# Kernel optimization log

Measured on AMD Instinct MI355X. Metric: run time of the kernel, lower is better.

The kernel has to match this reference:

```python
import jax, jax.numpy as jnp
import numpy as np

B, T, N, C, H = 32, 50, 1024, 128, 64


def setup_inputs() -> dict:
    key = jax.random.key(0)
    ks = jax.random.split(key, 5)
    s_ih = 1.0 / np.sqrt(H)
    return {
        "chars": jax.random.normal(ks[0], (B, T, N, C), dtype=jnp.float32),
        "W_ih": jax.random.uniform(ks[1], (3 * H, C), minval=-s_ih, maxval=s_ih, dtype=jnp.float32),
        "W_hh": jax.random.uniform(ks[2], (3 * H, H), minval=-s_ih, maxval=s_ih, dtype=jnp.float32),
        "b_ih": jax.random.uniform(ks[3], (3 * H,), minval=-s_ih, maxval=s_ih, dtype=jnp.float32),
        "b_hh": jax.random.uniform(ks[4], (3 * H,), minval=-s_ih, maxval=s_ih, dtype=jnp.float32),
    }


def _gru_scan(chars, W_ih, W_hh, b_ih, b_hh):
    b, t, n, c = chars.shape
    h_dim = W_hh.shape[1]
    # (B,T,N,C) -> (T, B*N, C): every (batch, stock) pair is an independent sequence
    x = jnp.transpose(chars, (1, 0, 2, 3)).reshape(t, b * n, c)
    # precompute input projections for all steps: (T, B*N, 3H)
    gi = jnp.einsum("tbc,gc->tbg", x, W_ih) + b_ih

    def step(h, gi_t):
        gh = h @ W_hh.T + b_hh                      # (B*N, 3H)
        i_r, i_z, i_n = jnp.split(gi_t, 3, axis=-1)
        h_r, h_z, h_n = jnp.split(gh, 3, axis=-1)
        r = jax.nn.sigmoid(i_r + h_r)
        z = jax.nn.sigmoid(i_z + h_z)
        nn_ = jnp.tanh(i_n + r * h_n)
        h_new = (1.0 - z) * nn_ + z * h
        return h_new, None

    h0 = jnp.zeros((b * n, h_dim), dtype=chars.dtype)
    h_final, _ = jax.lax.scan(step, h0, gi)
    return h_final.reshape(b, n, h_dim)


def reference(chars, W_ih, W_hh, b_ih, b_hh):
    return _gru_scan(chars, W_ih, W_hh, b_ih, b_hh)
```

## Files before the change

### kernel.cpp

```cpp
#include <hip/hip_runtime.h>


typedef _Float16 half8 __attribute__((ext_vector_type(8)));
typedef float f32x4 __attribute__((ext_vector_type(4)));

constexpr int T_ = 50, N_ = 1024, C_ = 128, H_ = 64;
constexpr uint32_t WHH_OFF = 0;
constexpr uint32_t XB_OFF  = 24576;
constexpr uint32_t HB_OFF  = 32768;
constexpr int LDS_BYTES = 36864;

__global__ void prep_weights(const float* __restrict__ Wih, const float* __restrict__ Whh,
                             _Float16* __restrict__ w16) {
  int i = blockIdx.x * 256 + threadIdx.x;
  if (i < 192 * 128) w16[i] = (_Float16)Wih[i];
  if (i < 192 * 64)  w16[24576 + i] = (_Float16)Whh[i];
}

__device__ __forceinline__ float sigm(float x) {
  return __builtin_amdgcn_rcpf(1.f + __expf(-x));
}

__device__ __forceinline__ half8 cvt8(float4 lo, float4 hi) {
  half8 v;
  v[0] = (_Float16)lo.x; v[1] = (_Float16)lo.y;
  v[2] = (_Float16)lo.z; v[3] = (_Float16)lo.w;
  v[4] = (_Float16)hi.x; v[5] = (_Float16)hi.y;
  v[6] = (_Float16)hi.z; v[7] = (_Float16)hi.w;
  return v;
}

__global__ __launch_bounds__(256, 4) void gru_g4(
    const float* __restrict__ x, const _Float16* __restrict__ w16,
    const float* __restrict__ bih, const float* __restrict__ bhh,
    float* __restrict__ out)
{
  __shared__ __align__(16) char lds[LDS_BYTES];
  const int tid = threadIdx.x;
  const int wv = tid >> 6, lane = tid & 63;
  const int c = lane & 15, g = lane >> 4;
  const int jt = wv;
  const int seq0 = blockIdx.x * 16;
  const int b = seq0 >> 10, n0 = seq0 & (N_ - 1);

  {
    const _Float16* whh = w16 + 24576;
#pragma unroll
    for (int rep = 0; rep < 6; ++rep) {
      int i = tid + rep * 256;
      int row = i >> 3, gr = i & 7;
      uint32_t byte = (uint32_t)row * 128 + (uint32_t)((gr ^ (row & 7)) << 4);
      *(half8*)(lds + WHH_OFF + byte) = *(const half8*)(whh + i * 8);
    }
    half8 zz = {};
    *(half8*)(lds + HB_OFF + tid * 16) = zz;
  }

  half8 wr[3][4];
#pragma unroll
  for (int gate = 0; gate < 3; ++gate)
#pragma unroll
    for (int ks = 0; ks < 4; ++ks)
      wr[gate][ks] = *(const half8*)(w16 + (gate * 64 + jt * 16 + c) * 128 + ks * 32 + g * 8);

  const int j = jt * 16 + c;
  const float br   = bih[j] + bhh[j];
  const float bz   = bih[64 + j] + bhh[64 + j];
  const float bin_ = bih[128 + j];
  const float bhn_ = bhh[128 + j];

  float hr[4] = {0.f, 0.f, 0.f, 0.f};

  const int sseq = tid >> 4;
  const uint32_t xw_off = (uint32_t)sseq * 256 +
                          (uint32_t)(((tid & 15) ^ (sseq & 7)) << 4);
  const float* xbase = x + ((size_t)b * T_ * N_ + n0 + sseq) * C_ + (tid & 15) * 8;
  const size_t stepstride = (size_t)N_ * C_;

#define WHHB(gate, ks2) \
  (*(const half8*)(lds + WHH_OFF + (uint32_t)(((gate) * 64 + jt * 16 + c) * 128) + \
                   (uint32_t)((((ks2) * 4 + g) ^ (c & 7)) << 4)))
#define MFMA16(a, bf, acc) __builtin_amdgcn_mfma_f32_16x16x32_f16((a), (bf), (acc), 0, 0, 0)

  {
    float4 r0 = *(const float4*)(xbase);
    float4 r1 = *(const float4*)(xbase + 4);
    *(half8*)(lds + XB_OFF + xw_off) = cvt8(r0, r1);
  }
  float4 ra = *(const float4*)(xbase + stepstride);
  float4 rb = *(const float4*)(xbase + stepstride + 4);
  __syncthreads();

  for (int t = 0; t < T_; ++t) {
    const uint32_t xr  = XB_OFF + (uint32_t)(t & 1) * 4096;
    const uint32_t hrd = HB_OFF + (uint32_t)((t + 1) & 1) * 2048;
    const uint32_t hwr = HB_OFF + (uint32_t)(t & 1) * 2048;

    half8 xa[4];
#pragma unroll
    for (int ks = 0; ks < 4; ++ks)
      xa[ks] = *(const half8*)(lds + xr + (uint32_t)c * 256 +
                               (uint32_t)(((ks * 4 + g) ^ (c & 7)) << 4));
    half8 ha[2];
#pragma unroll
    for (int ks2 = 0; ks2 < 2; ++ks2)
      ha[ks2] = *(const half8*)(lds + hrd + (uint32_t)c * 128 +
                                (uint32_t)(((ks2 * 4 + g) ^ (c & 7)) << 4));

    f32x4 aR = {0.f, 0.f, 0.f, 0.f}, aZ = {0.f, 0.f, 0.f, 0.f};
    f32x4 aN = {0.f, 0.f, 0.f, 0.f}, aH = {0.f, 0.f, 0.f, 0.f};

#pragma unroll
    for (int ks = 0; ks < 4; ++ks) {
      aR = MFMA16(xa[ks], wr[0][ks], aR);
      aZ = MFMA16(xa[ks], wr[1][ks], aZ);
      aN = MFMA16(xa[ks], wr[2][ks], aN);
    }
#pragma unroll
    for (int ks2 = 0; ks2 < 2; ++ks2) {
      aR = MFMA16(ha[ks2], WHHB(0, ks2), aR);
      aZ = MFMA16(ha[ks2], WHHB(1, ks2), aZ);
      aH = MFMA16(ha[ks2], WHHB(2, ks2), aH);
    }

#pragma unroll
    for (int v = 0; v < 4; ++v) {
      const float r = sigm(aR[v] + br);
      const float z = sigm(aZ[v] + bz);
      const float np = aN[v] + bin_ + r * (aH[v] + bhn_);
      const float nn = 1.f - 2.f * __builtin_amdgcn_rcpf(__expf(2.f * np) + 1.f);
      const float hn = (1.f - z) * nn + z * hr[v];
      hr[v] = hn;
      const int seq = g * 4 + v;
      const uint32_t gr = (uint32_t)((jt * 2 + (c >> 3)) ^ (seq & 7));
      *(_Float16*)(lds + hwr + (uint32_t)seq * 128 + (gr << 4) +
                   (uint32_t)((c & 7) * 2)) = (_Float16)hn;
    }

    if (t + 1 < T_) {
      *(half8*)(lds + XB_OFF + (uint32_t)((t + 1) & 1) * 4096 + xw_off) = cvt8(ra, rb);
      const int tn2 = (t + 2 < T_) ? t + 2 : T_ - 1;
      const float* xp = xbase + (size_t)tn2 * stepstride;
      ra = *(const float4*)(xp);
      rb = *(const float4*)(xp + 4);
    }
    __syncthreads();
  }

#pragma unroll
  for (int v = 0; v < 4; ++v)
    out[(size_t)(seq0 + g * 4 + v) * H_ + j] = hr[v];
#undef WHHB
#undef MFMA16
}

extern "C" void kernel_launch(void* const* d_in, const int* in_sizes, int n_in,
                              void* d_out, int out_size, void* d_ws, size_t ws_size,
                              hipStream_t stream) {
  const float* chars = (const float*)d_in[0];
  const float* Wih   = (const float*)d_in[1];
  const float* Whh   = (const float*)d_in[2];
  const float* bih   = (const float*)d_in[3];
  const float* bhh   = (const float*)d_in[4];

  _Float16* w16 = (_Float16*)d_ws;

  prep_weights<<<96, 256, 0, stream>>>(Wih, Whh, w16);
  gru_g4<<<2048, 256, 0, stream>>>(chars, w16, bih, bhh, (float*)d_out);
}
```

Baseline: 216.2 us.

## Stream x tiles via global_load_lds ring buffer and keep W_hh in registers

Replaces the register-staged x prefetch with direct global-to-LDS async loads (global_load_lds) into a 4-deep ring of fp32 tiles, issued three steps ahead and synchronised with vmcnt waits plus a raw barrier. The fp16 conversion of x now happens after the LDS read rather than before the write. The recurrent W_hh fragments move from LDS into registers, which frees LDS for the larger fp32 ring. The goal is to hide HBM latency with a deeper pipeline and remove the VGPR round trip, at the cost of higher register pressure (launch bounds drop from 4 to 3 blocks) and twice the LDS read traffic for x.

```diff
diff --git a/kernel.cpp b/kernel.cpp
--- a/kernel.cpp
+++ b/kernel.cpp
@@ -5,9 +5,8 @@
 typedef float f32x4 __attribute__((ext_vector_type(4)));
 
 constexpr int T_ = 50, N_ = 1024, C_ = 128, H_ = 64;
-constexpr uint32_t WHH_OFF = 0;
-constexpr uint32_t XB_OFF  = 24576;
-constexpr uint32_t HB_OFF  = 32768;
+constexpr uint32_t XB_OFF = 0;
+constexpr uint32_t HB_OFF = 32768;
 constexpr int LDS_BYTES = 36864;
 
 __global__ void prep_weights(const float* __restrict__ Wih, const float* __restrict__ Whh,
@@ -30,7 +29,13 @@
   return v;
 }
 
-__global__ __launch_bounds__(256, 4) void gru_g4(
+__device__ __forceinline__ void glds16(const char* g, char* l) {
+  __builtin_amdgcn_global_load_lds(
+      (const __attribute__((address_space(1))) void*)g,
+      (__attribute__((address_space(3))) void*)l, 16, 0, 0);
+}
+
+__global__ __launch_bounds__(256, 3) void gru_glds(
     const float* __restrict__ x, const _Float16* __restrict__ w16,
     const float* __restrict__ bih, const float* __restrict__ bhh,
     float* __restrict__ out)
@@ -43,18 +48,7 @@
   const int seq0 = blockIdx.x * 16;
   const int b = seq0 >> 10, n0 = seq0 & (N_ - 1);
 
-  {
-    const _Float16* whh = w16 + 24576;
-#pragma unroll
-    for (int rep = 0; rep < 6; ++rep) {
-      int i = tid + rep * 256;
-      int row = i >> 3, gr = i & 7;
-      uint32_t byte = (uint32_t)row * 128 + (uint32_t)((gr ^ (row & 7)) << 4);
-      *(half8*)(lds + WHH_OFF + byte) = *(const half8*)(whh + i * 8);
-    }
-    half8 zz = {};
-    *(half8*)(lds + HB_OFF + tid * 16) = zz;
-  }
+  *(uint2*)(lds + HB_OFF + 2048 + tid * 8) = (uint2){0u, 0u};
 
   half8 wr[3][4];
 #pragma unroll
@@ -62,6 +56,13 @@
 #pragma unroll
     for (int ks = 0; ks < 4; ++ks)
       wr[gate][ks] = *(const half8*)(w16 + (gate * 64 + jt * 16 + c) * 128 + ks * 32 + g * 8);
+  half8 wf[3][2];
+  const _Float16* whh = w16 + 24576;
+#pragma unroll
+  for (int gate = 0; gate < 3; ++gate)
+#pragma unroll
+    for (int ks2 = 0; ks2 < 2; ++ks2)
+      wf[gate][ks2] = *(const half8*)(whh + (gate * 64 + jt * 16 + c) * 64 + ks2 * 32 + g * 8);
 
   const int j = jt * 16 + c;
   const float br   = bih[j] + bhh[j];
@@ -71,58 +72,66 @@
 
   float hr[4] = {0.f, 0.f, 0.f, 0.f};
 
-  const int sseq = tid >> 4;
-  const uint32_t xw_off = (uint32_t)sseq * 256 +
-                          (uint32_t)(((tid & 15) ^ (sseq & 7)) << 4);
-  const float* xbase = x + ((size_t)b * T_ * N_ + n0 + sseq) * C_ + (tid & 15) * 8;
-  const size_t stepstride = (size_t)N_ * C_;
+  uint32_t sofs[2];
+#pragma unroll
+  for (int i = 0; i < 2; ++i) {
+    const int s_d = 4 * wv + 2 * i + (lane >> 5);
+    const uint32_t gd = (uint32_t)((lane & 24) | ((lane & 7) ^ (s_d & 7)));
+    sofs[i] = (uint32_t)s_d * 512 + gd * 16;
+  }
+  const size_t tilestride = (size_t)N_ * C_ * 4;
+  const char* tile0 = (const char*)(x + ((size_t)b * T_ * N_ + n0) * C_);
 
-#define WHHB(gate, ks2) \
-  (*(const half8*)(lds + WHH_OFF + (uint32_t)(((gate) * 64 + jt * 16 + c) * 128) + \
-                   (uint32_t)((((ks2) * 4 + g) ^ (c & 7)) << 4)))
+#define ISSUE_X(tt)                                                         \
+  do {                                                                      \
+    const int tcl = ((tt) < T_) ? (tt) : T_ - 1;                            \
+    const char* tb = tile0 + (size_t)tcl * tilestride;                      \
+    char* ldb = lds + XB_OFF + (uint32_t)((tt) & 3) * 8192 + (uint32_t)wv * 2048; \
+    glds16(tb + sofs[0], ldb);                                              \
+    glds16(tb + sofs[1], ldb + 1024);                                       \
+  } while (0)
+
 #define MFMA16(a, bf, acc) __builtin_amdgcn_mfma_f32_16x16x32_f16((a), (bf), (acc), 0, 0, 0)
 
-  {
-    float4 r0 = *(const float4*)(xbase);
-    float4 r1 = *(const float4*)(xbase + 4);
-    *(half8*)(lds + XB_OFF + xw_off) = cvt8(r0, r1);
-  }
-  float4 ra = *(const float4*)(xbase + stepstride);
-  float4 rb = *(const float4*)(xbase + stepstride + 4);
-  __syncthreads();
+  ISSUE_X(0); ISSUE_X(1); ISSUE_X(2);
 
   for (int t = 0; t < T_; ++t) {
-    const uint32_t xr  = XB_OFF + (uint32_t)(t & 1) * 4096;
-    const uint32_t hrd = HB_OFF + (uint32_t)((t + 1) & 1) * 2048;
-    const uint32_t hwr = HB_OFF + (uint32_t)(t & 1) * 2048;
+    asm volatile("s_waitcnt vmcnt(4) lgkmcnt(0)" ::: "memory");
+    __builtin_amdgcn_s_barrier();
+    __builtin_amdgcn_sched_barrier(0);
 
-    half8 xa[4];
-#pragma unroll
-    for (int ks = 0; ks < 4; ++ks)
-      xa[ks] = *(const half8*)(lds + xr + (uint32_t)c * 256 +
-                               (uint32_t)(((ks * 4 + g) ^ (c & 7)) << 4));
+    ISSUE_X(t + 3);
+
+    const uint32_t hrb = HB_OFF + (uint32_t)((t + 1) & 1) * 2048;
     half8 ha[2];
 #pragma unroll
     for (int ks2 = 0; ks2 < 2; ++ks2)
-      ha[ks2] = *(const half8*)(lds + hrd + (uint32_t)c * 128 +
+      ha[ks2] = *(const half8*)(lds + hrb + (uint32_t)c * 128 +
                                 (uint32_t)(((ks2 * 4 + g) ^ (c & 7)) << 4));
 
     f32x4 aR = {0.f, 0.f, 0.f, 0.f}, aZ = {0.f, 0.f, 0.f, 0.f};
     f32x4 aN = {0.f, 0.f, 0.f, 0.f}, aH = {0.f, 0.f, 0.f, 0.f};
 
+    const uint32_t xrb = XB_OFF + (uint32_t)(t & 3) * 8192 + (uint32_t)c * 512;
 #pragma unroll
     for (int ks = 0; ks < 4; ++ks) {
-      aR = MFMA16(xa[ks], wr[0][ks], aR);
-      aZ = MFMA16(xa[ks], wr[1][ks], aZ);
-      aN = MFMA16(xa[ks], wr[2][ks], aN);
+      const float4 p0 = *(const float4*)(lds + xrb +
+                          (uint32_t)((ks * 8 + ((g * 2 + 0) ^ (c & 7))) << 4));
+      const float4 p1 = *(const float4*)(lds + xrb +
+                          (uint32_t)((ks * 8 + ((g * 2 + 1) ^ (c & 7))) << 4));
+      const half8 a = cvt8(p0, p1);
+      aR = MFMA16(a, wr[0][ks], aR);
+      aZ = MFMA16(a, wr[1][ks], aZ);
+      aN = MFMA16(a, wr[2][ks], aN);
     }
 #pragma unroll
     for (int ks2 = 0; ks2 < 2; ++ks2) {
-      aR = MFMA16(ha[ks2], WHHB(0, ks2), aR);
-      aZ = MFMA16(ha[ks2], WHHB(1, ks2), aZ);
-      aH = MFMA16(ha[ks2], WHHB(2, ks2), aH);
+      aR = MFMA16(ha[ks2], wf[0][ks2], aR);
+      aZ = MFMA16(ha[ks2], wf[1][ks2], aZ);
+      aH = MFMA16(ha[ks2], wf[2][ks2], aH);
     }
 
+    const uint32_t hwb = HB_OFF + (uint32_t)(t & 1) * 2048;
 #pragma unroll
     for (int v = 0; v < 4; ++v) {
       const float r = sigm(aR[v] + br);
@@ -132,25 +141,16 @@
       const float hn = (1.f - z) * nn + z * hr[v];
       hr[v] = hn;
       const int seq = g * 4 + v;
-      const uint32_t gr = (uint32_t)((jt * 2 + (c >> 3)) ^ (seq & 7));
-      *(_Float16*)(lds + hwr + (uint32_t)seq * 128 + (gr << 4) +
+      const uint32_t gl = (uint32_t)((jt * 2 + (c >> 3)) ^ (seq & 7));
+      *(_Float16*)(lds + hwb + (uint32_t)seq * 128 + (gl << 4) +
                    (uint32_t)((c & 7) * 2)) = (_Float16)hn;
     }
-
-    if (t + 1 < T_) {
-      *(half8*)(lds + XB_OFF + (uint32_t)((t + 1) & 1) * 4096 + xw_off) = cvt8(ra, rb);
-      const int tn2 = (t + 2 < T_) ? t + 2 : T_ - 1;
-      const float* xp = xbase + (size_t)tn2 * stepstride;
-      ra = *(const float4*)(xp);
-      rb = *(const float4*)(xp + 4);
-    }
-    __syncthreads();
   }
 
 #pragma unroll
   for (int v = 0; v < 4; ++v)
     out[(size_t)(seq0 + g * 4 + v) * H_ + j] = hr[v];
-#undef WHHB
+#undef ISSUE_X
 #undef MFMA16
 }
 
@@ -166,5 +166,5 @@
   _Float16* w16 = (_Float16*)d_ws;
 
   prep_weights<<<96, 256, 0, stream>>>(Wih, Whh, w16);
-  gru_g4<<<2048, 256, 0, stream>>>(chars, w16, bih, bhh, (float*)d_out);
+  gru_glds<<<2048, 256, 0, stream>>>(chars, w16, bih, bhh, (float*)d_out);
 }
```

Result: slower. 242.0 us (+12.0%).

## Deepen input prefetch to two steps and keep global loads in flight across barriers

Applied to the files above, without the earlier changes.

The time loop is unrolled by two and keeps two register sets of upcoming x data, so global loads are issued three steps ahead instead of two. Each step's fp16 x tile is now stored to LDS before the MFMAs rather than after the gate math. The full __syncthreads is replaced by an lgkmcnt wait plus s_barrier, so outstanding global loads are not drained at every step. MFMA sections run at raised wave priority. The aim is to hide HBM latency in this bandwidth-heavy stream, at the cost of more registers, which could pressure occupancy under launch bounds of 4.

```diff
diff --git a/kernel.cpp b/kernel.cpp
--- a/kernel.cpp
+++ b/kernel.cpp
@@ -30,7 +30,7 @@
   return v;
 }
 
-__global__ __launch_bounds__(256, 4) void gru_g4(
+__global__ __launch_bounds__(256, 4) void gru_d2p(
     const float* __restrict__ x, const _Float16* __restrict__ w16,
     const float* __restrict__ bih, const float* __restrict__ bhh,
     float* __restrict__ out)
@@ -89,67 +89,77 @@
   }
   float4 ra = *(const float4*)(xbase + stepstride);
   float4 rb = *(const float4*)(xbase + stepstride + 4);
+  float4 rc = *(const float4*)(xbase + 2 * stepstride);
+  float4 rd = *(const float4*)(xbase + 2 * stepstride + 4);
   __syncthreads();
 
-  for (int t = 0; t < T_; ++t) {
-    const uint32_t xr  = XB_OFF + (uint32_t)(t & 1) * 4096;
-    const uint32_t hrd = HB_OFF + (uint32_t)((t + 1) & 1) * 2048;
-    const uint32_t hwr = HB_OFF + (uint32_t)(t & 1) * 2048;
+#define GRU_STEP(t, RA, RB)                                                     \
+  do {                                                                          \
+    const uint32_t xr  = XB_OFF + (uint32_t)((t) & 1) * 4096;                   \
+    const uint32_t hrd = HB_OFF + (uint32_t)(((t) + 1) & 1) * 2048;             \
+    const uint32_t hwr = HB_OFF + (uint32_t)((t) & 1) * 2048;                   \
+    half8 xa[4];                                                                \
+    _Pragma("unroll")                                                           \
+    for (int ks = 0; ks < 4; ++ks)                                              \
+      xa[ks] = *(const half8*)(lds + xr + (uint32_t)c * 256 +                   \
+                               (uint32_t)(((ks * 4 + g) ^ (c & 7)) << 4));      \
+    half8 ha[2];                                                                \
+    _Pragma("unroll")                                                           \
+    for (int ks2 = 0; ks2 < 2; ++ks2)                                           \
+      ha[ks2] = *(const half8*)(lds + hrd + (uint32_t)c * 128 +                 \
+                                (uint32_t)(((ks2 * 4 + g) ^ (c & 7)) << 4));    \
+                 \
+    if ((t) + 1 < T_) {                                                         \
+      *(half8*)(lds + XB_OFF + (uint32_t)(((t) + 1) & 1) * 4096 + xw_off) =     \
+          cvt8(RA, RB);                                                         \
+      const int tn = ((t) + 3 < T_) ? (t) + 3 : T_ - 1;                         \
+      const float* xp = xbase + (size_t)tn * stepstride;                        \
+      RA = *(const float4*)(xp);                                                \
+      RB = *(const float4*)(xp + 4);                                            \
+    }                                                                           \
+    f32x4 aR = {0.f, 0.f, 0.f, 0.f}, aZ = {0.f, 0.f, 0.f, 0.f};                 \
+    f32x4 aN = {0.f, 0.f, 0.f, 0.f}, aH = {0.f, 0.f, 0.f, 0.f};                 \
+    __builtin_amdgcn_s_setprio(1);                                              \
+    _Pragma("unroll")                                                           \
+    for (int ks = 0; ks < 4; ++ks) {                                            \
+      aR = MFMA16(xa[ks], wr[0][ks], aR);                                       \
+      aZ = MFMA16(xa[ks], wr[1][ks], aZ);                                       \
+      aN = MFMA16(xa[ks], wr[2][ks], aN);                                       \
+    }                                                                           \
+    _Pragma("unroll")                                                           \
+    for (int ks2 = 0; ks2 < 2; ++ks2) {                                         \
+      aR = MFMA16(ha[ks2], WHHB(0, ks2), aR);                                   \
+      aZ = MFMA16(ha[ks2], WHHB(1, ks2), aZ);                                   \
+      aH = MFMA16(ha[ks2], WHHB(2, ks2), aH);                                   \
+    }                                                                           \
+    __builtin_amdgcn_s_setprio(0);                                              \
+    _Pragma("unroll")                                                           \
+    for (int v = 0; v < 4; ++v) {                                               \
+      const float r = sigm(aR[v] + br);                                         \
+      const float z = sigm(aZ[v] + bz);                                         \
+      const float np = aN[v] + bin_ + r * (aH[v] + bhn_);                       \
+      const float nn = 1.f - 2.f * __builtin_amdgcn_rcpf(__expf(2.f * np) + 1.f); \
+      const float hn = (1.f - z) * nn + z * hr[v];                              \
+      hr[v] = hn;                                                               \
+      const int seq = g * 4 + v;                                                \
+      const uint32_t gr = (uint32_t)((jt * 2 + (c >> 3)) ^ (seq & 7));          \
+      *(_Float16*)(lds + hwr + (uint32_t)seq * 128 + (gr << 4) +                \
+                   (uint32_t)((c & 7) * 2)) = (_Float16)hn;                     \
+    }                                                                           \
+                                 \
+    asm volatile("s_waitcnt lgkmcnt(0)" ::: "memory");                          \
+    __builtin_amdgcn_s_barrier();                                               \
+  } while (0)
 
-    half8 xa[4];
-#pragma unroll
-    for (int ks = 0; ks < 4; ++ks)
-      xa[ks] = *(const half8*)(lds + xr + (uint32_t)c * 256 +
-                               (uint32_t)(((ks * 4 + g) ^ (c & 7)) << 4));
-    half8 ha[2];
-#pragma unroll
-    for (int ks2 = 0; ks2 < 2; ++ks2)
-      ha[ks2] = *(const half8*)(lds + hrd + (uint32_t)c * 128 +
-                                (uint32_t)(((ks2 * 4 + g) ^ (c & 7)) << 4));
-
-    f32x4 aR = {0.f, 0.f, 0.f, 0.f}, aZ = {0.f, 0.f, 0.f, 0.f};
-    f32x4 aN = {0.f, 0.f, 0.f, 0.f}, aH = {0.f, 0.f, 0.f, 0.f};
-
-#pragma unroll
-    for (int ks = 0; ks < 4; ++ks) {
-      aR = MFMA16(xa[ks], wr[0][ks], aR);
-      aZ = MFMA16(xa[ks], wr[1][ks], aZ);
-      aN = MFMA16(xa[ks], wr[2][ks], aN);
-    }
-#pragma unroll
-    for (int ks2 = 0; ks2 < 2; ++ks2) {
-      aR = MFMA16(ha[ks2], WHHB(0, ks2), aR);
-      aZ = MFMA16(ha[ks2], WHHB(1, ks2), aZ);
-      aH = MFMA16(ha[ks2], WHHB(2, ks2), aH);
-    }
-
-#pragma unroll
-    for (int v = 0; v < 4; ++v) {
-      const float r = sigm(aR[v] + br);
-      const float z = sigm(aZ[v] + bz);
-      const float np = aN[v] + bin_ + r * (aH[v] + bhn_);
-      const float nn = 1.f - 2.f * __builtin_amdgcn_rcpf(__expf(2.f * np) + 1.f);
-      const float hn = (1.f - z) * nn + z * hr[v];
-      hr[v] = hn;
-      const int seq = g * 4 + v;
-      const uint32_t gr = (uint32_t)((jt * 2 + (c >> 3)) ^ (seq & 7));
-      *(_Float16*)(lds + hwr + (uint32_t)seq * 128 + (gr << 4) +
-                   (uint32_t)((c & 7) * 2)) = (_Float16)hn;
-    }
-
-    if (t + 1 < T_) {
-      *(half8*)(lds + XB_OFF + (uint32_t)((t + 1) & 1) * 4096 + xw_off) = cvt8(ra, rb);
-      const int tn2 = (t + 2 < T_) ? t + 2 : T_ - 1;
-      const float* xp = xbase + (size_t)tn2 * stepstride;
-      ra = *(const float4*)(xp);
-      rb = *(const float4*)(xp + 4);
-    }
-    __syncthreads();
+  for (int t = 0; t < T_; t += 2) {
+    GRU_STEP(t, ra, rb);
+    GRU_STEP(t + 1, rc, rd);
   }
 
 #pragma unroll
   for (int v = 0; v < 4; ++v)
     out[(size_t)(seq0 + g * 4 + v) * H_ + j] = hr[v];
+#undef GRU_STEP
 #undef WHHB
 #undef MFMA16
 }
@@ -166,5 +176,5 @@
   _Float16* w16 = (_Float16*)d_ws;
 
   prep_weights<<<96, 256, 0, stream>>>(Wih, Whh, w16);
-  gru_g4<<<2048, 256, 0, stream>>>(chars, w16, bih, bhh, (float*)d_out);
+  gru_d2p<<<2048, 256, 0, stream>>>(chars, w16, bih, bhh, (float*)d_out);
 }
```

Result: slower. 271.3 us (+25.5%).
